# Optimization experiments

Hardware: AMD Instinct MI355X
Metric: run time of the kernel (lower is better)

Reference implementation:

```python
import jax, jax.numpy as jnp
import numpy as np

B, T, D, H, HS = 2, 256, 2048, 32, 64
LORA, DLORA, ST = 32, 64, 66  # maa lora rank, decay lora rank, state rows (2+HS)
EPS = 1e-5


def setup_inputs() -> dict:
    key = jax.random.key(0)
    ks = jax.random.split(key, 24)
    n = lambda k, sh, s=0.02: (jax.random.normal(k, sh, jnp.float32) * s)
    u = lambda k, sh: jax.random.uniform(k, sh, jnp.float32)
    return {
        "x": jax.random.normal(ks[0], (B, T, D), jnp.float32),
        "state": jax.random.normal(ks[1], (B, ST, D), jnp.float32) * 0.1,
        "ln1_w": jnp.ones((D,), jnp.float32),
        "ln1_b": jnp.zeros((D,), jnp.float32),
        "time_maa_x": u(ks[2], (D,)),
        "time_maa_w1": n(ks[3], (D, 5 * LORA)),
        "time_maa_w2": n(ks[4], (5, LORA, D)),
        "time_maa_k": u(ks[5], (D,)),
        "time_maa_w": u(ks[6], (D,)),
        "time_maa_v": u(ks[7], (D,)),
        "time_maa_r": u(ks[8], (D,)),
        "time_maa_g": u(ks[9], (D,)),
        "time_decay": n(ks[10], (D,), 0.5),
        "time_decay_w1": n(ks[11], (D, DLORA)),
        "time_decay_w2": n(ks[12], (DLORA, D)),
        "time_faaaa": n(ks[13], (H, HS, 1), 0.1),
        "receptance_weight": n(ks[14], (D, D)),
        "key_weight": n(ks[15], (D, D)),
        "value_weight": n(ks[16], (D, D)),
        "output_weight": n(ks[17], (D, D)),
        "gate_weight": n(ks[18], (D, D)),
        "lnx_w": jnp.ones((D,), jnp.float32),
        "lnx_b": jnp.zeros((D,), jnp.float32),
        "i": 0,
    }


def reference(x, state, ln1_w, ln1_b, time_maa_x, time_maa_w1, time_maa_w2,
              time_maa_k, time_maa_w, time_maa_v, time_maa_r, time_maa_g,
              time_decay, time_decay_w1, time_decay_w2, time_faaaa,
              receptance_weight, key_weight, value_weight, output_weight,
              gate_weight, lnx_w, lnx_b, i):
    # forward() early-returns time_mixing(ln1(x), state, i)
    mu = x.mean(-1, keepdims=True)
    var = ((x - mu) ** 2).mean(-1, keepdims=True)
    x = (x - mu) * jax.lax.rsqrt(var + EPS) * ln1_w + ln1_b

    i1 = (2 + HS) * i + 1
    # token shift: sx[t] = x[t-1] - x[t], with state row i1 as x[-1]
    sx = jnp.concatenate([state[:, i1][:, None] - x[:, :1], x[:, :-1] - x[:, 1:]], axis=1)

    xxx = x + sx * time_maa_x
    t5 = jnp.tanh(xxx @ time_maa_w1).reshape(B, T, 5, LORA)
    xxx5 = jnp.einsum('btfr,frd->btfd', t5, time_maa_w2)          # [B,T,5,D]
    maa = jnp.stack([time_maa_k, time_maa_w, time_maa_v, time_maa_r, time_maa_g])  # [5,D]
    x5 = x[:, :, None] + sx[:, :, None] * (maa + xxx5)            # [B,T,5,D]

    k = (x5[:, :, 0] @ key_weight.T).reshape(B, T, H, HS)
    w = jnp.exp(-jnp.exp(time_decay + jnp.tanh(x5[:, :, 1] @ time_decay_w1) @ time_decay_w2)).reshape(B, T, H, HS)
    v = (x5[:, :, 2] @ value_weight.T).reshape(B, T, H, HS)
    r = (x5[:, :, 3] @ receptance_weight.T).reshape(B, T, H, HS)
    g = jax.nn.silu(x5[:, :, 4] @ gate_weight.T)                  # [B,T,D]

    kv = jnp.einsum('bthi,bthj->bthij', k, v)                     # [B,T,H,HS,HS]
    prev0 = state[:, i1 + 1:i1 + 1 + HS].reshape(B, H, HS, HS)

    def step(prev, xs):
        kv_t, w_t = xs
        return kv_t + w_t[..., None] * prev, prev  # emit state BEFORE update

    _, state_s = jax.lax.scan(step, prev0,
                              (kv.transpose(1, 0, 2, 3, 4), w.transpose(1, 0, 2, 3)))
    state_s = state_s.transpose(1, 0, 2, 3, 4)                    # [B,T,H,HS,HS]

    wkv = time_faaaa * kv + state_s
    rwkv = jnp.einsum('bthj,bthjd->bthd', r, wkv)                 # [B,T,H,HS]

    # GroupNorm(num_groups=H) over each head's HS channels
    gm = rwkv.mean(-1, keepdims=True)
    gv = ((rwkv - gm) ** 2).mean(-1, keepdims=True)
    normed = (rwkv - gm) * jax.lax.rsqrt(gv + EPS)
    normed = normed * lnx_w.reshape(H, HS) + lnx_b.reshape(H, HS)
    normed = normed.reshape(B, T, D)

    return (normed * g) @ output_weight.T
```

## Files before the change

kernel.cpp:

```cpp
#include <hip/hip_runtime.h>
#include <hip/hip_bf16.h>

typedef unsigned short u16;
typedef __attribute__((ext_vector_type(4))) float f32x4;
typedef __attribute__((ext_vector_type(8))) short short8;
typedef __attribute__((ext_vector_type(4))) short bf16x4;

#define B_ 2
#define T_ 256
#define D_ 2048
#define H_ 32
#define HS_ 64
#define M_ 512
#define ST_ 66
#define EPS_ 1e-5f
#define NC_ 16
#define CL_ 16

__device__ __forceinline__ float bf2f(u16 u) {
    union { unsigned int i; float f; } c; c.i = ((unsigned int)u) << 16; return c.f;
}
__device__ __forceinline__ u16 f2bf(float f) {
    union { unsigned int i; float f; } c; c.f = f;
    unsigned int r = c.i + 0x7fffu + ((c.i >> 16) & 1u);
    return (u16)(r >> 16);
}
__device__ __forceinline__ u16 f2bf_hw(float f) {
    __hip_bfloat16 b = __float2bfloat16(f);
    return *reinterpret_cast<u16*>(&b);
}

__device__ __forceinline__ void gld16(const u16* g, u16* l) {
    __builtin_amdgcn_global_load_lds((const __attribute__((address_space(1))) void*)g,
                                     (__attribute__((address_space(3))) void*)l, 16, 0, 0);
}

__global__ __launch_bounds__(256) void ln_kernel(const float* __restrict__ x, const float* __restrict__ w,
                                                 const float* __restrict__ bias, float* __restrict__ xln)
{
    const int row = blockIdx.x;
    const float* xr = x + (size_t)row * D_;
    float* orow = xln + (size_t)row * D_;
    const int t = threadIdx.x;
    f32x4 a0 = *(const f32x4*)(xr + t * 8);
    f32x4 a1 = *(const f32x4*)(xr + t * 8 + 4);
    float s = 0.f, q = 0.f;
#pragma unroll
    for (int i = 0; i < 4; i++) { s += a0[i] + a1[i]; q += a0[i]*a0[i] + a1[i]*a1[i]; }
#pragma unroll
    for (int off = 1; off < 64; off <<= 1) { s += __shfl_xor(s, off, 64); q += __shfl_xor(q, off, 64); }
    __shared__ float ls[4], lq[4];
    const int wid = t >> 6, lane = t & 63;
    if (lane == 0) { ls[wid] = s; lq[wid] = q; }
    __syncthreads();
    s = ls[0] + ls[1] + ls[2] + ls[3];
    q = lq[0] + lq[1] + lq[2] + lq[3];
    const float mu = s * (1.f / D_);
    const float var = q * (1.f / D_) - mu * mu;
    const float rs = rsqrtf(var + EPS_);
#pragma unroll
    for (int i = 0; i < 8; i++) {
        int d = t * 8 + i;
        float f = (i < 4) ? a0[i] : a1[i - 4];
        orow[d] = (f - mu) * rs * w[d] + bias[d];
    }
}

__global__ __launch_bounds__(256) void shift_kernel(const float* __restrict__ xln, const float* __restrict__ state,
                                                    const float* __restrict__ maax, const int* __restrict__ ip,
                                                    float* __restrict__ sx, u16* __restrict__ xxxb)
{
    const size_t gid = (size_t)blockIdx.x * 256 + threadIdx.x;
    const size_t e = gid * 4;
    const int row = (int)(e >> 11);
    const int d = (int)(e & 2047);
    const int tt = row & (T_ - 1);
    const int b = row >> 8;
    const float* prev;
    if (tt == 0) prev = state + ((size_t)b * ST_ + (size_t)(66 * ip[0] + 1)) * D_ + d;
    else         prev = xln + e - D_;
    f32x4 p = *(const f32x4*)prev;
    f32x4 c = *(const f32x4*)(xln + e);
    f32x4 mx = *(const f32x4*)(maax + d);
    f32x4 sv;
    bf16x4 xv;
#pragma unroll
    for (int i = 0; i < 4; i++) { sv[i] = p[i] - c[i]; xv[i] = (short)f2bf(c[i] + sv[i] * mx[i]); }
    *(f32x4*)(sx + e) = sv;
    *(bf16x4*)(xxxb + e) = xv;
}

__global__ __launch_bounds__(256) void txp_kernel(const float* __restrict__ in, u16* __restrict__ out,
                                                  int K, int N)
{
    __shared__ float tile[32][33];
    const int k0 = blockIdx.x * 32, n0 = blockIdx.y * 32;
    const int c = threadIdx.x & 31, r8 = threadIdx.x >> 5;
#pragma unroll
    for (int i = 0; i < 4; i++) {
        int r = r8 + i * 8;
        tile[r][c] = in[(size_t)(k0 + r) * N + (n0 + c)];
    }
    __syncthreads();
#pragma unroll
    for (int i = 0; i < 4; i++) {
        int r = r8 + i * 8;
        out[(size_t)(n0 + r) * K + (k0 + c)] = f2bf(tile[c][r]);
    }
}

template<bool TANH>
__global__ __launch_bounds__(512) void wdot_kernel(const u16* __restrict__ A, const u16* __restrict__ Wt,
                                                   float* __restrict__ C, int N)
{
    const int gw = (int)((blockIdx.x * 512 + threadIdx.x) >> 6);
    const int lane = threadIdx.x & 63;
    const int m = gw / N, n = gw - m * N;
    const u16* a = A + (size_t)m * D_ + lane * 8;
    const u16* w = Wt + (size_t)n * D_ + lane * 8;
    float acc = 0.f;
#pragma unroll
    for (int i = 0; i < 4; i++) {
        short8 av = *(const short8*)(a + i * 512);
        short8 wv = *(const short8*)(w + i * 512);
#pragma unroll
        for (int j = 0; j < 8; j++)
            acc = fmaf(bf2f((u16)av[j]), bf2f((u16)wv[j]), acc);
    }
#pragma unroll
    for (int off = 1; off < 64; off <<= 1) acc += __shfl_xor(acc, off, 64);
    if (lane == 0) C[gw] = TANH ? tanhf(acc) : acc;
}

__global__ __launch_bounds__(256) void maa2_kernel(const float* __restrict__ t5, const float* __restrict__ w2,
                                                   const float* __restrict__ xln, const float* __restrict__ sxp,
                                                   const float* __restrict__ mk, const float* __restrict__ mw,
                                                   const float* __restrict__ mv, const float* __restrict__ mr,
                                                   const float* __restrict__ mg, u16* __restrict__ x5)
{
    const int gid = blockIdx.x * 256 + threadIdx.x;
    const int d = gid & (D_ - 1);
    const int mg4 = gid >> 11;
    const size_t m0 = (size_t)mg4 * 4;
    float xl[4], sv[4];
#pragma unroll
    for (int mm = 0; mm < 4; mm++) {
        const size_t e = (m0 + mm) * D_ + d;
        xl[mm] = xln[e];
        sv[mm] = sxp[e];
    }
    const float* t5b = t5 + m0 * 160;
#pragma unroll
    for (int f = 0; f < 5; f++) {
        const float* maa = (f == 0) ? mk : (f == 1) ? mw : (f == 2) ? mv : (f == 3) ? mr : mg;
        const float mf = maa[d];
        const float* w2f = w2 + (size_t)f * 32 * D_ + d;
        float a0 = 0, a1 = 0, a2 = 0, a3 = 0;
#pragma unroll 8
        for (int r = 0; r < 32; r++) {
            const float wv = w2f[(size_t)r * D_];
            a0 = fmaf(t5b[f * 32 + r], wv, a0);
            a1 = fmaf(t5b[160 + f * 32 + r], wv, a1);
            a2 = fmaf(t5b[320 + f * 32 + r], wv, a2);
            a3 = fmaf(t5b[480 + f * 32 + r], wv, a3);
        }
        const float accs[4] = {a0, a1, a2, a3};
#pragma unroll
        for (int mm = 0; mm < 4; mm++) {
            const size_t e = (m0 + mm) * D_ + d;
            x5[(size_t)f * M_ * D_ + e] = f2bf(xl[mm] + sv[mm] * (mf + accs[mm]));
        }
    }
}

__global__ __launch_bounds__(256) void decay2_kernel(const float* __restrict__ td, const float* __restrict__ dw2,
                                                     const float* __restrict__ tdec, float* __restrict__ wout)
{
    const int gid = blockIdx.x * 256 + threadIdx.x;
    const int d = gid & (D_ - 1);
    const int mg4 = gid >> 11;
    const float* wp = dw2 + d;
    const float* tb = td + (size_t)mg4 * 4 * 64;
    float a0 = 0, a1 = 0, a2 = 0, a3 = 0;
#pragma unroll 8
    for (int r = 0; r < 64; r++) {
        float wv = wp[(size_t)r * D_];
        a0 = fmaf(tb[r], wv, a0);
        a1 = fmaf(tb[64 + r], wv, a1);
        a2 = fmaf(tb[128 + r], wv, a2);
        a3 = fmaf(tb[192 + r], wv, a3);
    }
    const float base = tdec[d];
    const float accs[4] = {a0, a1, a2, a3};
#pragma unroll
    for (int mm = 0; mm < 4; mm++)
        wout[((size_t)mg4 * 4 + mm) * D_ + d] = expf(-expf(base + accs[mm]));
}

__device__ __forceinline__ void gemm2p_body(const u16* __restrict__ A, const float* __restrict__ Wf,
                                            float* __restrict__ C, int m0, int n0, int k0, int KC)
{
    __shared__ u16 As[2][128 * 64];
    __shared__ u16 Bs[2][64 * 64];
    const int tid = threadIdx.x;
    const int lane = tid & 63;
    const int wvd = tid >> 6;
    const int wm = (wvd >> 1) * 64;
    const int wn = (wvd & 1) * 32;

    f32x4 acc[4][2];
#pragma unroll
    for (int i = 0; i < 4; i++)
#pragma unroll
        for (int j = 0; j < 2; j++) { acc[i][j][0]=0.f; acc[i][j][1]=0.f; acc[i][j][2]=0.f; acc[i][j][3]=0.f; }

    const int srow = tid >> 3;
    const int sw8  = (((tid & 7) ^ (srow & 7)) << 3);
    const u16* Ag = A + (size_t)(m0 + srow) * D_ + k0 + sw8;
    const int ldst = tid * 8;

    const int br  = tid >> 2;
    const int bc0 = (tid & 3) * 16;
    const float* Wg = Wf + (size_t)(n0 + br) * D_ + k0 + bc0;
    const int bb0 = bc0 >> 3;
    const int dst0 = br * 64 + ((bb0 ^ (br & 7)) << 3);
    const int dst1 = br * 64 + (((bb0 + 1) ^ (br & 7)) << 3);

    const int rsw = (lane & 7) << 3;
    const int colb = (lane >> 4) * 8;
    const int fr = lane & 15;

    f32x4 xa0, xa1, xa2, xa3;
    f32x4 xb0, xb1, xb2, xb3;

#define LOADB_A(kt) { xa0 = *(const f32x4*)(Wg + (kt));      xa1 = *(const f32x4*)(Wg + (kt) + 4);  \
                      xa2 = *(const f32x4*)(Wg + (kt) + 8);  xa3 = *(const f32x4*)(Wg + (kt) + 12); }
#define LOADB_B(kt) { xb0 = *(const f32x4*)(Wg + (kt));      xb1 = *(const f32x4*)(Wg + (kt) + 4);  \
                      xb2 = *(const f32x4*)(Wg + (kt) + 8);  xb3 = *(const f32x4*)(Wg + (kt) + 12); }
#define STAGEA_(bb, kt)                                                           \
    {                                                                             \
        _Pragma("unroll")                                                         \
        for (int i = 0; i < 4; i++)                                               \
            gld16(Ag + (size_t)(i * 32) * D_ + (kt), &As[bb][i * 2048 + ldst]);   \
    }
#define WRITEB_(bb, r0, r1, r2, r3)                                               \
    {                                                                             \
        short8 p0, p1;                                                            \
        _Pragma("unroll")                                                         \
        for (int j = 0; j < 4; j++) {                                             \
            p0[j]     = (short)f2bf_hw(r0[j]); p0[j + 4] = (short)f2bf_hw(r1[j]); \
            p1[j]     = (short)f2bf_hw(r2[j]); p1[j + 4] = (short)f2bf_hw(r3[j]); \
        }                                                                         \
        *(short8*)&Bs[bb][dst0] = p0;                                             \
        *(short8*)&Bs[bb][dst1] = p1;                                             \
    }
#define MFMA_(bb)                                                                 \
    {                                                                             \
        _Pragma("unroll")                                                         \
        for (int kk = 0; kk < 64; kk += 32) {                                     \
            const int c = (kk + colb) ^ rsw;                                      \
            short8 av[4], bv[2];                                                  \
            _Pragma("unroll")                                                     \
            for (int mi = 0; mi < 4; mi++)                                        \
                av[mi] = *(const short8*)&As[bb][(wm + mi * 16 + fr) * 64 + c];   \
            _Pragma("unroll")                                                     \
            for (int ni = 0; ni < 2; ni++)                                        \
                bv[ni] = *(const short8*)&Bs[bb][(wn + ni * 16 + fr) * 64 + c];   \
            _Pragma("unroll")                                                     \
            for (int mi = 0; mi < 4; mi++)                                        \
                _Pragma("unroll")                                                 \
                for (int ni = 0; ni < 2; ni++)                                    \
                    acc[mi][ni] = __builtin_amdgcn_mfma_f32_16x16x32_bf16(av[mi], bv[ni], acc[mi][ni], 0, 0, 0); \
        }                                                                         \
    }

    LOADB_A(0);
    STAGEA_(0, 0);
    for (int kt = 0; ; kt += 128) {
        {
            const bool m1 = kt + 64 < KC;
            if (m1) { LOADB_B(kt + 64); STAGEA_(1, kt + 64); }
            if (m1) asm volatile("s_waitcnt vmcnt(8)" ::: "memory");
            else    asm volatile("s_waitcnt vmcnt(0)" ::: "memory");
            WRITEB_(0, xa0, xa1, xa2, xa3);
            asm volatile("s_waitcnt lgkmcnt(0)" ::: "memory");
            __builtin_amdgcn_s_barrier();
            MFMA_(0);
            __builtin_amdgcn_s_barrier();
            if (!m1) break;
        }
        {
            const bool m2 = kt + 128 < KC;
            if (m2) { LOADB_A(kt + 128); STAGEA_(0, kt + 128); }
            if (m2) asm volatile("s_waitcnt vmcnt(8)" ::: "memory");
            else    asm volatile("s_waitcnt vmcnt(0)" ::: "memory");
            WRITEB_(1, xb0, xb1, xb2, xb3);
            asm volatile("s_waitcnt lgkmcnt(0)" ::: "memory");
            __builtin_amdgcn_s_barrier();
            MFMA_(1);
            __builtin_amdgcn_s_barrier();
            if (!m2) break;
        }
    }
#undef LOADB_A
#undef LOADB_B
#undef STAGEA_
#undef WRITEB_
#undef MFMA_
    const int cr = wm + (lane >> 4) * 4;
    const int cc = wn + fr;
#pragma unroll
    for (int mi = 0; mi < 4; mi++)
#pragma unroll
        for (int ni = 0; ni < 2; ni++)
#pragma unroll
            for (int j = 0; j < 4; j++)
                C[(size_t)(m0 + cr + mi * 16 + j) * D_ + (n0 + cc + ni * 16)] = acc[mi][ni][j];
}

__global__ __launch_bounds__(256) void gemm4g_kernel(const u16* __restrict__ x5, const float* __restrict__ Wk,
                                                     const float* __restrict__ Wv, const float* __restrict__ Wr,
                                                     const float* __restrict__ Wg, float* __restrict__ kvK,
                                                     float* __restrict__ kvV, float* __restrict__ kvR,
                                                     float* __restrict__ kvG)
{
    const int s = blockIdx.z;
    const u16* A = x5 + (size_t)(s == 0 ? 0 : s + 1) * M_ * D_;
    const float* W = (s == 0) ? Wk : (s == 1) ? Wv : (s == 2) ? Wr : Wg;
    float* C = (s == 0) ? kvK : (s == 1) ? kvV : (s == 2) ? kvR : kvG;
    gemm2p_body(A, W, C, blockIdx.y * 128, blockIdx.x * 64, 0, D_);
}

__global__ __launch_bounds__(256) void gemm1g_kernel(const u16* __restrict__ y, const float* __restrict__ wo,
                                                     float* __restrict__ out, float* __restrict__ p0,
                                                     float* __restrict__ p1, float* __restrict__ p2)
{
    const int ks = blockIdx.z;
    float* C = (ks == 0) ? out : (ks == 1) ? p0 : (ks == 2) ? p1 : p2;
    gemm2p_body(y, wo, C, blockIdx.y * 128, blockIdx.x * 64, ks * 512, 512);
}

__global__ __launch_bounds__(256) void add3_kernel(float* __restrict__ dst, const float* __restrict__ s0,
                                                   const float* __restrict__ s1, const float* __restrict__ s2)
{
    const size_t e = ((size_t)blockIdx.x * 256 + threadIdx.x) * 4;
    f32x4 d = *(const f32x4*)(dst + e);
    f32x4 a = *(const f32x4*)(s0 + e);
    f32x4 b = *(const f32x4*)(s1 + e);
    f32x4 c = *(const f32x4*)(s2 + e);
#pragma unroll
    for (int i = 0; i < 4; i++) d[i] += (a[i] + b[i]) + c[i];
    *(f32x4*)(dst + e) = d;
}

__global__ __launch_bounds__(512) void rec1_kernel(const float* __restrict__ rB, const float* __restrict__ kB,
                                                   const float* __restrict__ wB, const float* __restrict__ vB,
                                                   const float* __restrict__ fa, float* __restrict__ rwkv,
                                                   float* __restrict__ CS, float* __restrict__ RP,
                                                   float* __restrict__ PC)
{
    const int bx = blockIdx.x;
    const int c  = bx & (NC_ - 1);
    const int bh = bx >> 4;
    const int h = bh & 31, b = bh >> 5;
    const int tid = threadIdx.x;
    const int wv = tid >> 6, lane = tid & 63;
    const int wg = wv >> 2;
    const int jb = lane >> 3, dsub = lane & 7;
    const int jbase = jb * 8;
    const int d0 = wg * 32 + (wv & 3) * 8 + dsub;

    __shared__ float stage[4][CL_][64];
    __shared__ float p2[CL_][8][64];
    __shared__ float p1[CL_][8];
    __shared__ float rpS[CL_ * 64];

    float S[8], pv[8], faj[8];
#pragma unroll
    for (int q = 0; q < 8; q++) { S[q] = 0.f; pv[q] = 1.f; faj[q] = fa[h * 64 + jbase + q]; }

    const size_t base = ((size_t)b * T_ * H_ + h) * HS_;
    const int t0 = c * CL_;
    const int arr = wv & 3;
    const float* mysrc = (arr == 0) ? rB : (arr == 1) ? kB : (arr == 2) ? wB : vB;
    const int ts0 = wg * 8 + (lane >> 4);
    const int sch = (lane & 15) * 4;
    const bool p1w = (wv == 0 && dsub == 0);

#pragma unroll
    for (int p = 0; p < 2; p++) {
        f32x4 v = *(const f32x4*)(mysrc + base + (size_t)(t0 + ts0 + p * 4) * (H_ * HS_) + sch);
        *(f32x4*)&stage[arr][ts0 + p * 4][sch] = v;
    }
    __syncthreads();

    f32x4 r0 = *(const f32x4*)&stage[0][0][jbase];
    f32x4 r1 = *(const f32x4*)&stage[0][0][jbase + 4];
    f32x4 k0 = *(const f32x4*)&stage[1][0][jbase];
    f32x4 k1 = *(const f32x4*)&stage[1][0][jbase + 4];
    f32x4 w0 = *(const f32x4*)&stage[2][0][jbase];
    f32x4 w1 = *(const f32x4*)&stage[2][0][jbase + 4];
    float vd = stage[3][0][d0];
#pragma unroll
    for (int ts = 0; ts < CL_; ++ts) {
        f32x4 nr0 = r0, nr1 = r1, nk0 = k0, nk1 = k1, nw0 = w0, nw1 = w1;
        float nvd = vd;
        if (ts + 1 < CL_) {
            nr0 = *(const f32x4*)&stage[0][ts + 1][jbase];
            nr1 = *(const f32x4*)&stage[0][ts + 1][jbase + 4];
            nk0 = *(const f32x4*)&stage[1][ts + 1][jbase];
            nk1 = *(const f32x4*)&stage[1][ts + 1][jbase + 4];
            nw0 = *(const f32x4*)&stage[2][ts + 1][jbase];
            nw1 = *(const f32x4*)&stage[2][ts + 1][jbase + 4];
            nvd = stage[3][ts + 1][d0];
        }
        float s1 = 0.f, s2 = 0.f;
#pragma unroll
        for (int q = 0; q < 4; q++) {
            s1 = fmaf(r0[q] * faj[q],     k0[q], s1);
            s1 = fmaf(r1[q] * faj[q + 4], k1[q], s1);
            s2 = fmaf(r0[q], S[q],     s2);
            s2 = fmaf(r1[q], S[q + 4], s2);
        }
        p2[ts][jb][d0 ^ (jb << 3)] = s2;
        if (p1w) {
            p1[ts][jb] = s1;
#pragma unroll
            for (int q = 0; q < 4; q++) {
                rpS[ts * 64 + jbase + q]     = r0[q] * pv[q];
                rpS[ts * 64 + jbase + 4 + q] = r1[q] * pv[q + 4];
            }
        }
#pragma unroll
        for (int q = 0; q < 4; q++) {
            pv[q]     *= w0[q];
            pv[q + 4] *= w1[q];
            S[q]       = fmaf(w0[q], S[q],     k0[q] * vd);
            S[q + 4]   = fmaf(w1[q], S[q + 4], k1[q] * vd);
        }
        r0 = nr0; r1 = nr1; k0 = nk0; k1 = nk1; w0 = nw0; w1 = nw1; vd = nvd;
    }
    __syncthreads();
#pragma unroll
    for (int p = 0; p < 2; p++) {
        const int ts = wv * 2 + p;
        f32x4 p1a = *(const f32x4*)&p1[ts][0];
        f32x4 p1b = *(const f32x4*)&p1[ts][4];
        float s1t = ((p1a[0] + p1a[1]) + (p1a[2] + p1a[3])) +
                    ((p1b[0] + p1b[1]) + (p1b[2] + p1b[3]));
        float s2t = 0.f;
#pragma unroll
        for (int j = 0; j < 8; j++) s2t += p2[ts][j][lane ^ (j << 3)];
        const float vvv = stage[3][ts][lane];
        rwkv[base + (size_t)(t0 + ts) * (H_ * HS_) + lane] = fmaf(vvv, s1t, s2t);
    }
    RP[(size_t)bx * (CL_ * 64) + tid]       = rpS[tid];
    RP[(size_t)bx * (CL_ * 64) + 512 + tid] = rpS[512 + tid];
#pragma unroll
    for (int q = 0; q < 8; q++)
        CS[(size_t)bx * 4096 + (size_t)(jbase + q) * 64 + d0] = S[q];
    if (p1w) {
#pragma unroll
        for (int q = 0; q < 8; q++)
            PC[(size_t)bx * 64 + jbase + q] = pv[q];
    }
}

__global__ __launch_bounds__(512) void rec2_kernel(const float* __restrict__ state, const int* __restrict__ ip,
                                                   float* __restrict__ CS, const float* __restrict__ PC)
{
    const int bh = blockIdx.x;
    const int b = bh >> 5, h = bh & 31;
    const int tid = threadIdx.x;
    const int o = tid * 8;
    const int jrow = tid >> 3;
    const float* Sp = state + (size_t)b * ST_ * D_ + (size_t)(66 * ip[0] + 2) * D_ + (size_t)h * HS_ * HS_;
    f32x4 c0 = *(const f32x4*)(Sp + o);
    f32x4 c1 = *(const f32x4*)(Sp + o + 4);
    for (int c = 0; c < NC_; ++c) {
        float* cs = CS + ((size_t)(bh * NC_ + c)) * 4096 + o;
        f32x4 l0 = *(const f32x4*)cs;
        f32x4 l1 = *(const f32x4*)(cs + 4);
        const float pc = PC[(size_t)(bh * NC_ + c) * 64 + jrow];
        f32x4 n0, n1;
#pragma unroll
        for (int i = 0; i < 4; i++) { n0[i] = fmaf(pc, c0[i], l0[i]); n1[i] = fmaf(pc, c1[i], l1[i]); }
        *(f32x4*)cs = c0;
        *(f32x4*)(cs + 4) = c1;
        c0 = n0; c1 = n1;
    }
}

__global__ __launch_bounds__(256) void rec3gn_kernel(const float* __restrict__ CS, const float* __restrict__ RP,
                                                     const float* __restrict__ rwkv, const float* __restrict__ gpre,
                                                     const float* __restrict__ lnxw, const float* __restrict__ lnxb,
                                                     u16* __restrict__ y)
{
    const int bx = blockIdx.x;
    const int c  = bx & (NC_ - 1);
    const int bh = bx >> 4;
    const int h = bh & 31, b = bh >> 5;
    const int tid = threadIdx.x;
    __shared__ float Ss[4096];
    __shared__ float rp[CL_ * 64];
#pragma unroll
    for (int i = 0; i < 4; i++)
        *(f32x4*)&Ss[tid * 4 + i * 1024] = *(const f32x4*)(CS + (size_t)bx * 4096 + tid * 4 + i * 1024);
    *(f32x4*)&rp[tid * 4] = *(const f32x4*)(RP + (size_t)bx * (CL_ * 64) + tid * 4);
    __syncthreads();
    const int tl = tid >> 4;
    const int d4 = (tid & 15) * 4;
    f32x4 acc; acc[0] = acc[1] = acc[2] = acc[3] = 0.f;
    const float* rpr = &rp[tl * 64];
#pragma unroll 16
    for (int j = 0; j < 64; ++j) {
        const float rv = rpr[j];
        const f32x4 sv = *(const f32x4*)&Ss[j * 64 + d4];
#pragma unroll
        for (int i = 0; i < 4; i++) acc[i] = fmaf(rv, sv[i], acc[i]);
    }
    const size_t base = ((size_t)b * T_ * H_ + h) * HS_;
    const size_t eb = base + (size_t)(c * CL_ + tl) * (H_ * HS_);
    const f32x4 cur = *(const f32x4*)(rwkv + eb + d4);
    f32x4 val;
#pragma unroll
    for (int i = 0; i < 4; i++) val[i] = cur[i] + acc[i];
    float s = 0.f, q = 0.f;
#pragma unroll
    for (int i = 0; i < 4; i++) { s += val[i]; q += val[i] * val[i]; }
#pragma unroll
    for (int off = 1; off < 16; off <<= 1) { s += __shfl_xor(s, off, 64); q += __shfl_xor(q, off, 64); }
    const float mu = s * (1.f / 64.f);
    const float var = q * (1.f / 64.f) - mu * mu;
    const float rs = rsqrtf(var + EPS_);
    bf16x4 yv;
#pragma unroll
    for (int i = 0; i < 4; i++) {
        const int hj = h * 64 + d4 + i;
        const float nrm = (val[i] - mu) * rs * lnxw[hj] + lnxb[hj];
        const float gp = gpre[eb + d4 + i];
        const float gv = gp / (1.f + expf(-gp));
        yv[i] = (short)f2bf(nrm * gv);
    }
    *(bf16x4*)(y + eb + d4) = yv;
}

extern "C" void kernel_launch(void* const* d_in, const int* in_sizes, int n_in,
                              void* d_out, int out_size, void* d_ws, size_t ws_size,
                              hipStream_t stream)
{
    const float* x     = (const float*)d_in[0];
    const float* state = (const float*)d_in[1];
    const float* ln1w  = (const float*)d_in[2];
    const float* ln1b  = (const float*)d_in[3];
    const float* maax  = (const float*)d_in[4];
    const float* w1    = (const float*)d_in[5];
    const float* w2    = (const float*)d_in[6];
    const float* maak  = (const float*)d_in[7];
    const float* maaw  = (const float*)d_in[8];
    const float* maav  = (const float*)d_in[9];
    const float* maar  = (const float*)d_in[10];
    const float* maag  = (const float*)d_in[11];
    const float* tdec  = (const float*)d_in[12];
    const float* dw1   = (const float*)d_in[13];
    const float* dw2   = (const float*)d_in[14];
    const float* fa    = (const float*)d_in[15];
    const float* wrec  = (const float*)d_in[16];
    const float* wkey  = (const float*)d_in[17];
    const float* wval  = (const float*)d_in[18];
    const float* wout  = (const float*)d_in[19];
    const float* wgate = (const float*)d_in[20];
    const float* lnxw  = (const float*)d_in[21];
    const float* lnxb  = (const float*)d_in[22];
    const int*   ip    = (const int*)d_in[23];

    char* ws = (char*)d_ws;
    const size_t MD = (size_t)M_ * D_;
    float* CS   = (float*)(ws);
    float* RP   = (float*)(ws + ((size_t)16 << 20));
    float* PC   = (float*)(ws + ((size_t)20 << 20));
    float* xln  = (float*)(ws + ((size_t)40 << 20));
    float* sx   = (float*)(ws + ((size_t)44 << 20));
    u16*   xxxb = (u16*)  (ws + ((size_t)48 << 20));
    u16*   w1t  = (u16*)  (ws + ((size_t)50 << 20));
    u16*   dw1t = (u16*)  (ws + ((size_t)51 << 20));
    float* t5   = (float*)(ws + ((size_t)52 << 20));
    float* td   = (float*)(ws + ((size_t)53 << 20));
    u16*   x5   = (u16*)  (ws + ((size_t)54 << 20));
    float* wdec = (float*)(ws + ((size_t)64 << 20));
    float* kvK  = (float*)(ws + ((size_t)40 << 20));
    float* kvV  = (float*)(ws + ((size_t)44 << 20));
    float* kvR  = (float*)(ws + ((size_t)48 << 20));
    float* kvG  = (float*)(ws + ((size_t)68 << 20));
    float* rwkv = (float*)(ws + ((size_t)72 << 20));
    u16*   y    = (u16*)  (ws + ((size_t)76 << 20));
    float* pp0  = (float*)(ws + ((size_t)54 << 20));
    float* pp1  = (float*)(ws + ((size_t)58 << 20));
    float* pp2  = (float*)(ws + ((size_t)62 << 20));
    float* out  = (float*)d_out;

    hipLaunchKernelGGL(ln_kernel,     dim3(512),      dim3(256), 0, stream, x, ln1w, ln1b, xln);
    hipLaunchKernelGGL(shift_kernel,  dim3(1024),     dim3(256), 0, stream, xln, state, maax, ip, sx, xxxb);
    hipLaunchKernelGGL(txp_kernel,    dim3(64, 5),    dim3(256), 0, stream, w1, w1t, D_, 160);
    hipLaunchKernelGGL(txp_kernel,    dim3(64, 2),    dim3(256), 0, stream, dw1, dw1t, D_, 64);
    hipLaunchKernelGGL((wdot_kernel<true>), dim3(10240), dim3(512), 0, stream, xxxb, w1t, t5, 160);
    hipLaunchKernelGGL(maa2_kernel,   dim3(1024),     dim3(256), 0, stream, t5, w2, xln, sx, maak, maaw, maav, maar, maag, x5);
    hipLaunchKernelGGL((wdot_kernel<true>), dim3(4096), dim3(512), 0, stream, x5 + MD, dw1t, td, 64);
    hipLaunchKernelGGL(decay2_kernel, dim3(1024),     dim3(256), 0, stream, td, dw2, tdec, wdec);
    hipLaunchKernelGGL(gemm4g_kernel, dim3(32, 4, 4), dim3(256), 0, stream, x5, wkey, wval, wrec, wgate, kvK, kvV, kvR, kvG);
    hipLaunchKernelGGL(rec1_kernel,   dim3(B_ * H_ * NC_), dim3(512), 0, stream, kvR, kvK, wdec, kvV, fa, rwkv, CS, RP, PC);
    hipLaunchKernelGGL(rec2_kernel,   dim3(B_ * H_),  dim3(512), 0, stream, state, ip, CS, PC);
    hipLaunchKernelGGL(rec3gn_kernel, dim3(B_ * H_ * NC_), dim3(256), 0, stream, CS, RP, rwkv, kvG, lnxw, lnxb, y);
    hipLaunchKernelGGL(gemm1g_kernel, dim3(32, 4, 4), dim3(256), 0, stream, y, wout, out, pp0, pp1, pp2);
    hipLaunchKernelGGL(add3_kernel,   dim3(1024),     dim3(256), 0, stream, out, pp0, pp1, pp2);

    (void)in_sizes; (void)n_in; (void)out_size; (void)ws_size;
}
```

Baseline: 182.4 us.

## Halve GEMM K-tile to 32 and add split-K to projection and output GEMMs

Shrinks the shared GEMM body's K-tile from 64 to 32, halving LDS use and the per-stage loads. The four-way K/V/R/G projection GEMM is split into two K halves (grid z goes from 4 to 8), and a new add kernel reduces the partial results. The output GEMM goes from 4-way to 8-way split-K with a 7-partial reduction kernel. The aim is more blocks for better occupancy and CU fill, at the cost of extra partial-sum memory traffic, one more launch and more barriers per K step.

```diff
diff --git a/kernel.cpp b/kernel.cpp
--- a/kernel.cpp
+++ b/kernel.cpp
@@ -200,8 +200,8 @@
 __device__ __forceinline__ void gemm2p_body(const u16* __restrict__ A, const float* __restrict__ Wf,
                                             float* __restrict__ C, int m0, int n0, int k0, int KC)
 {
-    __shared__ u16 As[2][128 * 64];
-    __shared__ u16 Bs[2][64 * 64];
+    __shared__ u16 As[2][128 * 32];
+    __shared__ u16 Bs[2][64 * 32];
     const int tid = threadIdx.x;
     const int lane = tid & 63;
     const int wvd = tid >> 6;
@@ -214,75 +214,63 @@
 #pragma unroll
         for (int j = 0; j < 2; j++) { acc[i][j][0]=0.f; acc[i][j][1]=0.f; acc[i][j][2]=0.f; acc[i][j][3]=0.f; }
 
-    const int srow = tid >> 3;
-    const int sw8  = (((tid & 7) ^ (srow & 7)) << 3);
-    const u16* Ag = A + (size_t)(m0 + srow) * D_ + k0 + sw8;
+    const int srow = tid >> 2;
+    const int schk = tid & 3;
+    const u16* Ag = A + (size_t)(m0 + srow) * D_ + k0 + ((schk ^ (srow & 3)) << 3);
     const int ldst = tid * 8;
 
-    const int br  = tid >> 2;
-    const int bc0 = (tid & 3) * 16;
-    const float* Wg = Wf + (size_t)(n0 + br) * D_ + k0 + bc0;
-    const int bb0 = bc0 >> 3;
-    const int dst0 = br * 64 + ((bb0 ^ (br & 7)) << 3);
-    const int dst1 = br * 64 + (((bb0 + 1) ^ (br & 7)) << 3);
-
-    const int rsw = (lane & 7) << 3;
-    const int colb = (lane >> 4) * 8;
+    const int br = srow;
+    const float* Wg = Wf + (size_t)(n0 + br) * D_ + k0 + schk * 8;
+    const int bdst = br * 32 + (((schk) ^ (br & 3)) << 3);
+
     const int fr = lane & 15;
-
-    f32x4 xa0, xa1, xa2, xa3;
-    f32x4 xb0, xb1, xb2, xb3;
-
-#define LOADB_A(kt) { xa0 = *(const f32x4*)(Wg + (kt));      xa1 = *(const f32x4*)(Wg + (kt) + 4);  \
-                      xa2 = *(const f32x4*)(Wg + (kt) + 8);  xa3 = *(const f32x4*)(Wg + (kt) + 12); }
-#define LOADB_B(kt) { xb0 = *(const f32x4*)(Wg + (kt));      xb1 = *(const f32x4*)(Wg + (kt) + 4);  \
-                      xb2 = *(const f32x4*)(Wg + (kt) + 8);  xb3 = *(const f32x4*)(Wg + (kt) + 12); }
+    const int rchk = ((lane >> 4) ^ (fr & 3)) << 3;
+
+    f32x4 xa0, xa1;
+    f32x4 xb0, xb1;
+
+#define LOADB_A(kt) { xa0 = *(const f32x4*)(Wg + (kt)); xa1 = *(const f32x4*)(Wg + (kt) + 4); }
+#define LOADB_B(kt) { xb0 = *(const f32x4*)(Wg + (kt)); xb1 = *(const f32x4*)(Wg + (kt) + 4); }
 #define STAGEA_(bb, kt)                                                           \
     {                                                                             \
-        _Pragma("unroll")                                                         \
-        for (int i = 0; i < 4; i++)                                               \
-            gld16(Ag + (size_t)(i * 32) * D_ + (kt), &As[bb][i * 2048 + ldst]);   \
-    }
-#define WRITEB_(bb, r0, r1, r2, r3)                                               \
+        gld16(Ag + (kt), &As[bb][ldst]);                                          \
+        gld16(Ag + (size_t)64 * D_ + (kt), &As[bb][2048 + ldst]);                 \
+    }
+#define WRITEB_(bb, r0, r1)                                                       \
     {                                                                             \
-        short8 p0, p1;                                                            \
+        short8 p0;                                                                \
         _Pragma("unroll")                                                         \
         for (int j = 0; j < 4; j++) {                                             \
-            p0[j]     = (short)f2bf_hw(r0[j]); p0[j + 4] = (short)f2bf_hw(r1[j]); \
-            p1[j]     = (short)f2bf_hw(r2[j]); p1[j + 4] = (short)f2bf_hw(r3[j]); \
+            p0[j]     = (short)f2bf_hw(r0[j]);                                    \
+            p0[j + 4] = (short)f2bf_hw(r1[j]);                                    \
         }                                                                         \
-        *(short8*)&Bs[bb][dst0] = p0;                                             \
-        *(short8*)&Bs[bb][dst1] = p1;                                             \
+        *(short8*)&Bs[bb][bdst] = p0;                                             \
     }
 #define MFMA_(bb)                                                                 \
     {                                                                             \
+        short8 av[4], bv[2];                                                      \
         _Pragma("unroll")                                                         \
-        for (int kk = 0; kk < 64; kk += 32) {                                     \
-            const int c = (kk + colb) ^ rsw;                                      \
-            short8 av[4], bv[2];                                                  \
-            _Pragma("unroll")                                                     \
-            for (int mi = 0; mi < 4; mi++)                                        \
-                av[mi] = *(const short8*)&As[bb][(wm + mi * 16 + fr) * 64 + c];   \
+        for (int mi = 0; mi < 4; mi++)                                            \
+            av[mi] = *(const short8*)&As[bb][(wm + mi * 16 + fr) * 32 + rchk];    \
+        _Pragma("unroll")                                                         \
+        for (int ni = 0; ni < 2; ni++)                                            \
+            bv[ni] = *(const short8*)&Bs[bb][(wn + ni * 16 + fr) * 32 + rchk];    \
+        _Pragma("unroll")                                                         \
+        for (int mi = 0; mi < 4; mi++)                                            \
             _Pragma("unroll")                                                     \
             for (int ni = 0; ni < 2; ni++)                                        \
-                bv[ni] = *(const short8*)&Bs[bb][(wn + ni * 16 + fr) * 64 + c];   \
-            _Pragma("unroll")                                                     \
-            for (int mi = 0; mi < 4; mi++)                                        \
-                _Pragma("unroll")                                                 \
-                for (int ni = 0; ni < 2; ni++)                                    \
-                    acc[mi][ni] = __builtin_amdgcn_mfma_f32_16x16x32_bf16(av[mi], bv[ni], acc[mi][ni], 0, 0, 0); \
-        }                                                                         \
+                acc[mi][ni] = __builtin_amdgcn_mfma_f32_16x16x32_bf16(av[mi], bv[ni], acc[mi][ni], 0, 0, 0); \
     }
 
     LOADB_A(0);
     STAGEA_(0, 0);
-    for (int kt = 0; ; kt += 128) {
+    for (int kt = 0; ; kt += 64) {
         {
-            const bool m1 = kt + 64 < KC;
-            if (m1) { LOADB_B(kt + 64); STAGEA_(1, kt + 64); }
-            if (m1) asm volatile("s_waitcnt vmcnt(8)" ::: "memory");
+            const bool m1 = kt + 32 < KC;
+            if (m1) { LOADB_B(kt + 32); STAGEA_(1, kt + 32); }
+            if (m1) asm volatile("s_waitcnt vmcnt(4)" ::: "memory");
             else    asm volatile("s_waitcnt vmcnt(0)" ::: "memory");
-            WRITEB_(0, xa0, xa1, xa2, xa3);
+            WRITEB_(0, xa0, xa1);
             asm volatile("s_waitcnt lgkmcnt(0)" ::: "memory");
             __builtin_amdgcn_s_barrier();
             MFMA_(0);
@@ -290,11 +278,11 @@
             if (!m1) break;
         }
         {
-            const bool m2 = kt + 128 < KC;
-            if (m2) { LOADB_A(kt + 128); STAGEA_(0, kt + 128); }
-            if (m2) asm volatile("s_waitcnt vmcnt(8)" ::: "memory");
+            const bool m2 = kt + 64 < KC;
+            if (m2) { LOADB_A(kt + 64); STAGEA_(0, kt + 64); }
+            if (m2) asm volatile("s_waitcnt vmcnt(4)" ::: "memory");
             else    asm volatile("s_waitcnt vmcnt(0)" ::: "memory");
-            WRITEB_(1, xb0, xb1, xb2, xb3);
+            WRITEB_(1, xb0, xb1);
             asm volatile("s_waitcnt lgkmcnt(0)" ::: "memory");
             __builtin_amdgcn_s_barrier();
             MFMA_(1);
@@ -322,34 +310,50 @@
                                                      const float* __restrict__ Wv, const float* __restrict__ Wr,
                                                      const float* __restrict__ Wg, float* __restrict__ kvK,
                                                      float* __restrict__ kvV, float* __restrict__ kvR,
-                                                     float* __restrict__ kvG)
-{
-    const int s = blockIdx.z;
+                                                     float* __restrict__ kvG, float* __restrict__ pp4)
+{
+    const int s  = blockIdx.z >> 1;
+    const int ks = blockIdx.z & 1;
     const u16* A = x5 + (size_t)(s == 0 ? 0 : s + 1) * M_ * D_;
     const float* W = (s == 0) ? Wk : (s == 1) ? Wv : (s == 2) ? Wr : Wg;
-    float* C = (s == 0) ? kvK : (s == 1) ? kvV : (s == 2) ? kvR : kvG;
-    gemm2p_body(A, W, C, blockIdx.y * 128, blockIdx.x * 64, 0, D_);
-}
-
-__global__ __launch_bounds__(256) void gemm1g_kernel(const u16* __restrict__ y, const float* __restrict__ wo,
-                                                     float* __restrict__ out, float* __restrict__ p0,
-                                                     float* __restrict__ p1, float* __restrict__ p2)
-{
-    const int ks = blockIdx.z;
-    float* C = (ks == 0) ? out : (ks == 1) ? p0 : (ks == 2) ? p1 : p2;
-    gemm2p_body(y, wo, C, blockIdx.y * 128, blockIdx.x * 64, ks * 512, 512);
-}
-
-__global__ __launch_bounds__(256) void add3_kernel(float* __restrict__ dst, const float* __restrict__ s0,
-                                                   const float* __restrict__ s1, const float* __restrict__ s2)
-{
+    float* C = (ks == 0) ? ((s == 0) ? kvK : (s == 1) ? kvV : (s == 2) ? kvR : kvG)
+                         : pp4 + (size_t)s * M_ * D_;
+    gemm2p_body(A, W, C, blockIdx.y * 128, blockIdx.x * 64, ks * 1024, 1024);
+}
+
+__global__ __launch_bounds__(256) void add4g_kernel(float* __restrict__ dk, float* __restrict__ dv,
+                                                    float* __restrict__ dr, float* __restrict__ dg,
+                                                    const float* __restrict__ pp4)
+{
+    const int s = blockIdx.y;
+    float* dst = (s == 0) ? dk : (s == 1) ? dv : (s == 2) ? dr : dg;
     const size_t e = ((size_t)blockIdx.x * 256 + threadIdx.x) * 4;
     f32x4 d = *(const f32x4*)(dst + e);
-    f32x4 a = *(const f32x4*)(s0 + e);
-    f32x4 b = *(const f32x4*)(s1 + e);
-    f32x4 c = *(const f32x4*)(s2 + e);
-#pragma unroll
-    for (int i = 0; i < 4; i++) d[i] += (a[i] + b[i]) + c[i];
+    f32x4 a = *(const f32x4*)(pp4 + (size_t)s * M_ * D_ + e);
+#pragma unroll
+    for (int i = 0; i < 4; i++) d[i] += a[i];
+    *(f32x4*)(dst + e) = d;
+}
+
+__global__ __launch_bounds__(256) void gemm1g_kernel(const u16* __restrict__ y, const float* __restrict__ wo,
+                                                     float* __restrict__ out, float* __restrict__ pp1)
+{
+    const int ks = blockIdx.z;
+    float* C = (ks == 0) ? out : pp1 + (size_t)(ks - 1) * M_ * D_;
+    gemm2p_body(y, wo, C, blockIdx.y * 128, blockIdx.x * 64, ks * 256, 256);
+}
+
+__global__ __launch_bounds__(256) void add7_kernel(float* __restrict__ dst, const float* __restrict__ pp1)
+{
+    const size_t e = ((size_t)blockIdx.x * 256 + threadIdx.x) * 4;
+    const size_t MD = (size_t)M_ * D_;
+    f32x4 d = *(const f32x4*)(dst + e);
+#pragma unroll
+    for (int i = 0; i < 7; i++) {
+        f32x4 a = *(const f32x4*)(pp1 + (size_t)i * MD + e);
+#pragma unroll
+        for (int j = 0; j < 4; j++) d[j] += a[j];
+    }
     *(f32x4*)(dst + e) = d;
 }
 
@@ -576,9 +580,11 @@
 
     char* ws = (char*)d_ws;
     const size_t MD = (size_t)M_ * D_;
+    float* pp4  = (float*)(ws);
     float* CS   = (float*)(ws);
     float* RP   = (float*)(ws + ((size_t)16 << 20));
     float* PC   = (float*)(ws + ((size_t)20 << 20));
+    float* pp1  = (float*)(ws);
     float* xln  = (float*)(ws + ((size_t)40 << 20));
     float* sx   = (float*)(ws + ((size_t)44 << 20));
     u16*   xxxb = (u16*)  (ws + ((size_t)48 << 20));
@@ -594,9 +600,6 @@
     float* kvG  = (float*)(ws + ((size_t)68 << 20));
     float* rwkv = (float*)(ws + ((size_t)72 << 20));
     u16*   y    = (u16*)  (ws + ((size_t)76 << 20));
-    float* pp0  = (float*)(ws + ((size_t)54 << 20));
-    float* pp1  = (float*)(ws + ((size_t)58 << 20));
-    float* pp2  = (float*)(ws + ((size_t)62 << 20));
     float* out  = (float*)d_out;
 
     hipLaunchKernelGGL(ln_kernel,     dim3(512),      dim3(256), 0, stream, x, ln1w, ln1b, xln);
@@ -607,12 +610,13 @@
     hipLaunchKernelGGL(maa2_kernel,   dim3(1024),     dim3(256), 0, stream, t5, w2, xln, sx, maak, maaw, maav, maar, maag, x5);
     hipLaunchKernelGGL((wdot_kernel<true>), dim3(4096), dim3(512), 0, stream, x5 + MD, dw1t, td, 64);
     hipLaunchKernelGGL(decay2_kernel, dim3(1024),     dim3(256), 0, stream, td, dw2, tdec, wdec);
-    hipLaunchKernelGGL(gemm4g_kernel, dim3(32, 4, 4), dim3(256), 0, stream, x5, wkey, wval, wrec, wgate, kvK, kvV, kvR, kvG);
+    hipLaunchKernelGGL(gemm4g_kernel, dim3(32, 4, 8), dim3(256), 0, stream, x5, wkey, wval, wrec, wgate, kvK, kvV, kvR, kvG, pp4);
+    hipLaunchKernelGGL(add4g_kernel,  dim3(1024, 4),  dim3(256), 0, stream, kvK, kvV, kvR, kvG, pp4);
     hipLaunchKernelGGL(rec1_kernel,   dim3(B_ * H_ * NC_), dim3(512), 0, stream, kvR, kvK, wdec, kvV, fa, rwkv, CS, RP, PC);
     hipLaunchKernelGGL(rec2_kernel,   dim3(B_ * H_),  dim3(512), 0, stream, state, ip, CS, PC);
     hipLaunchKernelGGL(rec3gn_kernel, dim3(B_ * H_ * NC_), dim3(256), 0, stream, CS, RP, rwkv, kvG, lnxw, lnxb, y);
-    hipLaunchKernelGGL(gemm1g_kernel, dim3(32, 4, 4), dim3(256), 0, stream, y, wout, out, pp0, pp1, pp2);
-    hipLaunchKernelGGL(add3_kernel,   dim3(1024),     dim3(256), 0, stream, out, pp0, pp1, pp2);
+    hipLaunchKernelGGL(gemm1g_kernel, dim3(32, 4, 8), dim3(256), 0, stream, y, wout, out, pp1);
+    hipLaunchKernelGGL(add7_kernel,   dim3(1024),     dim3(256), 0, stream, out, pp1);
 
     (void)in_sizes; (void)n_in; (void)out_size; (void)ws_size;
 }
```

After: 195.9 us. 1.07x slower.
